# Kernel tuning notes

Measured on AMD Instinct MI355X. Metric: run time of the kernel, lower is better.

## Reference

```python
import jax, jax.numpy as jnp
import numpy as np

D3D, D2D, DTEXT, DPROJ, SEQ_LEN = 256, 768, 3072, 3072, 256
B, S, T = 32, 256, 512


def setup_inputs() -> dict:
    key = jax.random.key(0)
    ks = jax.random.split(key, 9)
    s3 = 1.0 / np.sqrt(D3D)
    s2 = 1.0 / np.sqrt(D2D)
    sf = 1.0 / np.sqrt(DPROJ * 3)
    return {
        "feat_3d": jax.random.normal(ks[0], (B, D3D), jnp.float32),
        "feat_2d": jax.random.normal(ks[1], (B, S, D2D), jnp.float32),
        "feat_text": jax.random.normal(ks[2], (B, T, DTEXT), jnp.float32),
        "W3d": jax.random.uniform(ks[3], (DPROJ, D3D), jnp.float32, -s3, s3),
        "b3d": jax.random.uniform(ks[4], (DPROJ,), jnp.float32, -s3, s3),
        "W2d": jax.random.uniform(ks[5], (DPROJ, D2D), jnp.float32, -s2, s2),
        "b2d": jax.random.uniform(ks[6], (DPROJ,), jnp.float32, -s2, s2),
        "Wf": jax.random.uniform(ks[7], (DPROJ, DPROJ * 3), jnp.float32, -sf, sf),
        "bf": jax.random.uniform(ks[8], (DPROJ,), jnp.float32, -sf, sf),
    }


def reference(feat_3d, feat_2d, feat_text, W3d, b3d, W2d, b2d, Wf, bf):
    # Projections
    f3p = feat_3d @ W3d.T + b3d                      # [B, P]
    f2p = jnp.einsum("bsd,pd->bsp", feat_2d, W2d) + b2d  # [B, S, P]

    # Attention pooling of 2D slice features against global 3D feature
    scores_s = jnp.einsum("bsp,bp->bs", f2p, f3p)    # [B, S]
    w_s = jax.nn.softmax(scores_s, axis=1)
    pooled_2d = jnp.einsum("bs,bsp->bp", w_s, f2p)   # [B, P]

    # Attention pooling of text features against global 3D feature
    scores_t = jnp.einsum("btp,bp->bt", feat_text, f3p)  # [B, T]
    w_t = jax.nn.softmax(scores_t, axis=1)
    pooled_text = jnp.einsum("bt,btp->bp", w_t, feat_text)  # [B, P]

    # All seq_len rows of the original's concatenated input are identical,
    # so compute the fusion GEMM once per batch element and broadcast.
    fused_vec = jnp.concatenate([f3p, pooled_2d, pooled_text], axis=-1) @ Wf.T + bf  # [B, P]
    return jnp.broadcast_to(fused_vec[:, None, :], (fused_vec.shape[0], SEQ_LEN, fused_vec.shape[1]))
```

## Files before the change

### kernel.cpp

```cpp
#include <hip/hip_runtime.h>

#define NB 32
#define NS 256
#define NT 512
#define KD3 256
#define KD2 768
#define NP 3072
#define KFZ 9216

__device__ __forceinline__ float wave_red_sum(float v) {
#pragma unroll
  for (int o = 32; o; o >>= 1) v += __shfl_xor(v, o, 64);
  return v;
}
__device__ __forceinline__ float wave_red_max(float v) {
#pragma unroll
  for (int o = 32; o; o >>= 1) v = fmaxf(v, __shfl_xor(v, o, 64));
  return v;
}

__global__ __launch_bounds__(256) void k1_f3p(const float* __restrict__ f3d,
                                              const float* __restrict__ W3d,
                                              const float* __restrict__ b3d,
                                              float* __restrict__ c0, float* __restrict__ c1,
                                              float* __restrict__ c2, float* __restrict__ c3) {
  int b = blockIdx.x & 31, pc = blockIdx.x >> 5;
  __shared__ float4 xs[KD3 / 4];
  int tid = threadIdx.x;
  if (tid < KD3 / 4) xs[tid] = ((const float4*)(f3d + b * KD3))[tid];
  __syncthreads();
  int p = pc * 256 + tid;
  const float4* wrow = (const float4*)(W3d + (size_t)p * KD3);
  float acc = b3d[p];
#pragma unroll 8
  for (int i = 0; i < KD3 / 4; ++i) {
    float4 w = wrow[i], x = xs[i];
    acc = fmaf(w.x, x.x, acc); acc = fmaf(w.y, x.y, acc);
    acc = fmaf(w.z, x.z, acc); acc = fmaf(w.w, x.w, acc);
  }
  size_t o = (size_t)b * KFZ + p;
  c0[o] = acc; c1[o] = 0.f; c2[o] = 0.f; c3[o] = 0.f;
}

__global__ __launch_bounds__(256) void k_L2(const float* __restrict__ ftx,
                                            const float* __restrict__ W2d,
                                            const float* __restrict__ c0,
                                            float* __restrict__ g_part,
                                            float* __restrict__ Pt,
                                            float* __restrict__ ml) {
  __shared__ float4 smem4[768];
  float* sm = (float*)smem4;
  int tid = threadIdx.x;
  if (blockIdx.x < 512) {
    int b = blockIdx.x & 31, tch = blockIdx.x >> 5;
    for (int i = tid; i < NP / 4; i += 256)
      smem4[i] = ((const float4*)(c0 + (size_t)b * KFZ))[i];
    __syncthreads();
    int wave = tid >> 6, lane = tid & 63;
    int t0 = tch * 32 + wave * 8;
    float m = -3.0e38f, l = 0.f;
    float4 acc[12];
#pragma unroll
    for (int j = 0; j < 12; ++j) acc[j] = make_float4(0.f, 0.f, 0.f, 0.f);
    for (int r = 0; r < 8; ++r) {
      const float4* row = (const float4*)(ftx + ((size_t)(b * NT + t0 + r)) * NP);
      float4 xr[12];
#pragma unroll
      for (int j = 0; j < 12; ++j) xr[j] = row[lane + 64 * j];
      float s = 0.f;
#pragma unroll
      for (int j = 0; j < 12; ++j) {
        float4 f = smem4[lane + 64 * j];
        s = fmaf(xr[j].x, f.x, s); s = fmaf(xr[j].y, f.y, s);
        s = fmaf(xr[j].z, f.z, s); s = fmaf(xr[j].w, f.w, s);
      }
      s = wave_red_sum(s);
      float mn = fmaxf(m, s);
      float al = __expf(m - mn);
      float e = __expf(s - mn);
      l = fmaf(l, al, e);
#pragma unroll
      for (int j = 0; j < 12; ++j) {
        acc[j].x = fmaf(acc[j].x, al, e * xr[j].x);
        acc[j].y = fmaf(acc[j].y, al, e * xr[j].y);
        acc[j].z = fmaf(acc[j].z, al, e * xr[j].z);
        acc[j].w = fmaf(acc[j].w, al, e * xr[j].w);
      }
      m = mn;
    }
    int c = tch * 4 + wave;
    float4* Pr = (float4*)(Pt + (size_t)(c * NB + b) * NP);
#pragma unroll
    for (int j = 0; j < 12; ++j) Pr[lane + 64 * j] = acc[j];
    if (lane == 0) { ml[(c * NB + b) * 2] = m; ml[(c * NB + b) * 2 + 1] = l; }
  } else {
    int id = blockIdx.x - 512;
    int dc = id % 3, kc = id / 3;
    int p0 = kc * 96;
    for (int i = tid; i < NB * 96; i += 256) {
      int bb = i / 96, pp = i - bb * 96;
      sm[i] = c0[(size_t)bb * KFZ + p0 + pp];
    }
    __syncthreads();
    int d = dc * 256 + tid;
    float acc[NB];
#pragma unroll
    for (int b = 0; b < NB; ++b) acc[b] = 0.f;
    for (int pp = 0; pp < 96; pp += 4) {
      float w0 = W2d[(size_t)(p0 + pp + 0) * KD2 + d];
      float w1 = W2d[(size_t)(p0 + pp + 1) * KD2 + d];
      float w2 = W2d[(size_t)(p0 + pp + 2) * KD2 + d];
      float w3 = W2d[(size_t)(p0 + pp + 3) * KD2 + d];
#pragma unroll
      for (int b = 0; b < NB; ++b) {
        float4 x4 = *(const float4*)&sm[b * 96 + pp];
        acc[b] = fmaf(w0, x4.x, acc[b]); acc[b] = fmaf(w1, x4.y, acc[b]);
        acc[b] = fmaf(w2, x4.z, acc[b]); acc[b] = fmaf(w3, x4.w, acc[b]);
      }
    }
#pragma unroll
    for (int b = 0; b < NB; ++b) g_part[(size_t)(kc * NB + b) * KD2 + d] = acc[b];
  }
}

__global__ __launch_bounds__(256) void k_L3(const float* __restrict__ f2d,
                                            const float* __restrict__ g_part,
                                            float* __restrict__ sraw,
                                            const float* __restrict__ Pt,
                                            const float* __restrict__ ml,
                                            float* __restrict__ c0, float* __restrict__ c1,
                                            float* __restrict__ c2, float* __restrict__ c3) {
  __shared__ float4 sh4[KD2 / 4];
  float* sh = (float*)sh4;
  int tid = threadIdx.x;
  if (blockIdx.x < 128) {
    int b = blockIdx.x & 31, sc = blockIdx.x >> 5;
    for (int i = tid; i < KD2; i += 256) {
      float a = 0.f;
      for (int c = 0; c < 32; ++c) a += g_part[(size_t)(c * NB + b) * KD2 + i];
      sh[i] = a;
    }
    __syncthreads();
    int wave = tid >> 6, lane = tid & 63;
    for (int i = 0; i < 16; ++i) {
      int s = sc * 64 + wave * 16 + i;
      const float4* row = (const float4*)(f2d + ((size_t)b * NS + s) * KD2);
      float acc = 0.f;
#pragma unroll
      for (int j = 0; j < 3; ++j) {
        float4 v = row[lane + 64 * j];
        float4 g = sh4[lane + 64 * j];
        acc = fmaf(v.x, g.x, acc); acc = fmaf(v.y, g.y, acc);
        acc = fmaf(v.z, g.z, acc); acc = fmaf(v.w, g.w, acc);
      }
      acc = wave_red_sum(acc);
      if (lane == 0) sraw[b * NS + s] = acc;
    }
  } else {
    int id = blockIdx.x - 128;
    int b = id & 31, pc = id >> 5;
    if (tid < 64) {
      sh[2 * tid] = ml[(tid * NB + b) * 2];
      sh[2 * tid + 1] = ml[(tid * NB + b) * 2 + 1];
    }
    __syncthreads();
    float M = -3.0e38f;
    for (int c = 0; c < 64; ++c) M = fmaxf(M, sh[2 * c]);
    float denom = 0.f;
    for (int c = 0; c < 64; ++c) denom += __expf(sh[2 * c] - M) * sh[2 * c + 1];
    float inv = 1.f / denom;
    int p4 = pc * 1024 + tid * 4;
    float4 a = make_float4(0.f, 0.f, 0.f, 0.f);
    for (int c = 0; c < 64; ++c) {
      float w = __expf(sh[2 * c] - M);
      float4 v = *(const float4*)&Pt[(size_t)(c * NB + b) * NP + p4];
      a.x = fmaf(w, v.x, a.x); a.y = fmaf(w, v.y, a.y);
      a.z = fmaf(w, v.z, a.z); a.w = fmaf(w, v.w, a.w);
    }
    a.x *= inv; a.y *= inv; a.z *= inv; a.w *= inv;
    size_t o = (size_t)b * KFZ + 2 * NP + p4;
    float4 z = make_float4(0.f, 0.f, 0.f, 0.f);
    *(float4*)&c0[o] = a;
    *(float4*)&c1[o] = z; *(float4*)&c2[o] = z; *(float4*)&c3[o] = z;
  }
}

__global__ __launch_bounds__(256) void k3c_sm(const float* __restrict__ f2d,
                                              const float* __restrict__ sraw,
                                              float* __restrict__ p2f) {
  int b = blockIdx.x & 31;
  int r = blockIdx.x >> 5;
  int dc = r % 3, sc = r / 3;
  __shared__ float pr[NS];
  __shared__ float red[8];
  int tid = threadIdx.x;
  int wave = tid >> 6, lane = tid & 63;
  float v = sraw[b * NS + tid];
  float mx = wave_red_max(v);
  if (lane == 0) red[wave] = mx;
  __syncthreads();
  float M = fmaxf(fmaxf(red[0], red[1]), fmaxf(red[2], red[3]));
  float e = __expf(v - M);
  pr[tid] = e;
  float smv = wave_red_sum(e);
  if (lane == 0) red[4 + wave] = smv;
  __syncthreads();
  float inv = 1.f / (red[4] + red[5] + red[6] + red[7]);
  int d = dc * 256 + tid;
  float acc = 0.f;
  const float* base = f2d + ((size_t)b * NS + sc * 128) * KD2 + d;
#pragma unroll 8
  for (int s = 0; s < 128; ++s)
    acc = fmaf(pr[sc * 128 + s], base[(size_t)s * KD2], acc);
  p2f[(size_t)(sc * NB + b) * KD2 + d] = acc * inv;
}

__global__ __launch_bounds__(256) void k5_pool2d(const float* __restrict__ W2d,
                                                 const float* __restrict__ b2d,
                                                 const float* __restrict__ p2f,
                                                 float* __restrict__ c0, float* __restrict__ c1,
                                                 float* __restrict__ c2, float* __restrict__ c3) {
  int pb = blockIdx.x >> 2, ks = blockIdx.x & 3;
  __shared__ __align__(16) float wt[64 * 68];
  __shared__ __align__(16) float xt[32 * 68];
  int tid = threadIdx.x;
  int tp = tid & 31, tb = tid >> 5;
  float acc[2][4];
#pragma unroll
  for (int i = 0; i < 2; ++i)
#pragma unroll
    for (int j = 0; j < 4; ++j) acc[i][j] = 0.f;
  for (int dk = 0; dk < 3; ++dk) {
    int d0 = ks * 192 + dk * 64;
#pragma unroll
    for (int it = 0; it < 4; ++it) {
      int idx = tid + it * 256;
      int row = idx >> 4, c4 = (idx & 15) * 4;
      *(float4*)&wt[row * 68 + c4] =
          *(const float4*)&W2d[(size_t)(pb * 64 + row) * KD2 + d0 + c4];
    }
#pragma unroll
    for (int it = 0; it < 2; ++it) {
      int idx = tid + it * 256;
      int row = idx >> 4, c4 = (idx & 15) * 4;
      float4 a = *(const float4*)&p2f[(size_t)row * KD2 + d0 + c4];
      float4 bq = *(const float4*)&p2f[(size_t)(NB + row) * KD2 + d0 + c4];
      a.x += bq.x; a.y += bq.y; a.z += bq.z; a.w += bq.w;
      *(float4*)&xt[row * 68 + c4] = a;
    }
    __syncthreads();
#pragma unroll 4
    for (int kk = 0; kk < 64; kk += 4) {
      float4 wv[2], xv[4];
#pragma unroll
      for (int i = 0; i < 2; ++i) wv[i] = *(const float4*)&wt[(tp + 32 * i) * 68 + kk];
#pragma unroll
      for (int j = 0; j < 4; ++j) xv[j] = *(const float4*)&xt[(tb + 8 * j) * 68 + kk];
#pragma unroll
      for (int i = 0; i < 2; ++i)
#pragma unroll
        for (int j = 0; j < 4; ++j) {
          acc[i][j] = fmaf(wv[i].x, xv[j].x, acc[i][j]);
          acc[i][j] = fmaf(wv[i].y, xv[j].y, acc[i][j]);
          acc[i][j] = fmaf(wv[i].z, xv[j].z, acc[i][j]);
          acc[i][j] = fmaf(wv[i].w, xv[j].w, acc[i][j]);
        }
    }
    __syncthreads();
  }
  float* dst = (ks == 0) ? c0 : (ks == 1) ? c1 : (ks == 2) ? c2 : c3;
#pragma unroll
  for (int i = 0; i < 2; ++i) {
    int p = pb * 64 + tp + 32 * i;
    float bias = (ks == 0) ? b2d[p] : 0.f;
#pragma unroll
    for (int j = 0; j < 4; ++j)
      dst[(size_t)(tb + 8 * j) * KFZ + NP + p] = acc[i][j] + bias;
  }
}

__global__ __launch_bounds__(256) void k6_fused(const float* __restrict__ Wf,
                                                const float* __restrict__ c0,
                                                const float* __restrict__ c1,
                                                const float* __restrict__ c2,
                                                const float* __restrict__ c3,
                                                float* __restrict__ fpart) {
  int pb = blockIdx.x >> 4, kc = blockIdx.x & 15;
  __shared__ __align__(16) float wt[192 * 68];
  __shared__ __align__(16) float xt[32 * 68];
  int tid = threadIdx.x;
  int tp = tid & 31, tb = tid >> 5;
  float acc[6][4];
#pragma unroll
  for (int i = 0; i < 6; ++i)
#pragma unroll
    for (int j = 0; j < 4; ++j) acc[i][j] = 0.f;
  for (int kt = 0; kt < 9; ++kt) {
    int k0 = kc * 576 + kt * 64;
#pragma unroll
    for (int it = 0; it < 12; ++it) {
      int idx = tid + it * 256;
      int row = idx >> 4, c4 = (idx & 15) * 4;
      *(float4*)&wt[row * 68 + c4] =
          *(const float4*)&Wf[(size_t)(pb * 192 + row) * KFZ + k0 + c4];
    }
#pragma unroll
    for (int it = 0; it < 2; ++it) {
      int idx = tid + it * 256;
      int row = idx >> 4, c4 = (idx & 15) * 4;
      size_t o = (size_t)row * KFZ + k0 + c4;
      float4 a = *(const float4*)&c0[o];
      float4 v1 = *(const float4*)&c1[o];
      float4 v2 = *(const float4*)&c2[o];
      float4 v3 = *(const float4*)&c3[o];
      a.x += v1.x + v2.x + v3.x; a.y += v1.y + v2.y + v3.y;
      a.z += v1.z + v2.z + v3.z; a.w += v1.w + v2.w + v3.w;
      *(float4*)&xt[row * 68 + c4] = a;
    }
    __syncthreads();
#pragma unroll 4
    for (int kk = 0; kk < 64; kk += 4) {
      float4 wv[6], xv[4];
#pragma unroll
      for (int i = 0; i < 6; ++i) wv[i] = *(const float4*)&wt[(tp + 32 * i) * 68 + kk];
#pragma unroll
      for (int j = 0; j < 4; ++j) xv[j] = *(const float4*)&xt[(tb + 8 * j) * 68 + kk];
#pragma unroll
      for (int i = 0; i < 6; ++i)
#pragma unroll
        for (int j = 0; j < 4; ++j) {
          acc[i][j] = fmaf(wv[i].x, xv[j].x, acc[i][j]);
          acc[i][j] = fmaf(wv[i].y, xv[j].y, acc[i][j]);
          acc[i][j] = fmaf(wv[i].z, xv[j].z, acc[i][j]);
          acc[i][j] = fmaf(wv[i].w, xv[j].w, acc[i][j]);
        }
    }
    __syncthreads();
  }
#pragma unroll
  for (int i = 0; i < 6; ++i)
#pragma unroll
    for (int j = 0; j < 4; ++j)
      fpart[(size_t)(kc * NB + tb + 8 * j) * NP + pb * 192 + tp + 32 * i] = acc[i][j];
}

__global__ __launch_bounds__(256) void k7_bcast(const float* __restrict__ fpart,
                                                const float* __restrict__ bfv,
                                                float* __restrict__ out) {
  int b = blockIdx.x & 31;
  int r = blockIdx.x >> 5;
  int pc = r % 3, sc = r / 3;
  int tid = threadIdx.x;
  int p4 = pc * 1024 + 4 * tid;
  float4 v = *(const float4*)&bfv[p4];
#pragma unroll
  for (int c = 0; c < 16; ++c) {
    float4 a = *(const float4*)&fpart[(size_t)(c * NB + b) * NP + p4];
    v.x += a.x; v.y += a.y; v.z += a.z; v.w += a.w;
  }
  float* obase = out + (size_t)b * NS * NP + p4;
  for (int ss = 0; ss < 64; ++ss) {
    int s = sc * 64 + ss;
    *(float4*)(obase + (size_t)s * NP) = v;
  }
}

extern "C" void kernel_launch(void* const* d_in, const int* in_sizes, int n_in,
                              void* d_out, int out_size, void* d_ws, size_t ws_size,
                              hipStream_t stream) {
  const float* f3d = (const float*)d_in[0];
  const float* f2d = (const float*)d_in[1];
  const float* ftx = (const float*)d_in[2];
  const float* W3d = (const float*)d_in[3];
  const float* b3d = (const float*)d_in[4];
  const float* W2d = (const float*)d_in[5];
  const float* b2d = (const float*)d_in[6];
  const float* Wf  = (const float*)d_in[7];
  const float* bfv = (const float*)d_in[8];
  float* out = (float*)d_out;
  float* ws = (float*)d_ws;

  float* c0     = ws;
  float* c1     = ws + 294912;
  float* c2     = ws + 589824;
  float* c3     = ws + 884736;
  float* g_part = ws + 1179648;
  float* sraw   = ws + 1966080;
  float* p2f    = ws + 1974272;
  float* ml     = ws + 2023424;
  float* Pt     = ws + 2027520;
  float* fpart  = ws + 8318976;

  k1_f3p<<<384, 256, 0, stream>>>(f3d, W3d, b3d, c0, c1, c2, c3);
  k_L2<<<608, 256, 0, stream>>>(ftx, W2d, c0, g_part, Pt, ml);
  k_L3<<<224, 256, 0, stream>>>(f2d, g_part, sraw, Pt, ml, c0, c1, c2, c3);
  k3c_sm<<<192, 256, 0, stream>>>(f2d, sraw, p2f);
  k5_pool2d<<<192, 256, 0, stream>>>(W2d, b2d, p2f, c0, c1, c2, c3);
  k6_fused<<<256, 256, 0, stream>>>(Wf, c0, c1, c2, c3, fpart);
  k7_bcast<<<384, 256, 0, stream>>>(fpart, bfv, out);
}
```

Baseline: 553.1 us.

## Split fused kernels, double-buffer text rows, and raise grid sizes across stages

The two multi-role kernels are split into separate text-attention, g-partial, score, and combine kernels. The text kernel now double-buffers row loads in registers and uses split accumulators. The 2D pooling, fusion GEMM, and broadcast kernels get finer partitions, so each launches more blocks. A separate pass pre-sums the four partial buffers before the fusion GEMM. This trades more kernel launches and extra memory passes for better overlap of loads and more occupancy on each stage.

```diff
diff --git a/kernel.cpp b/kernel.cpp
--- a/kernel.cpp
+++ b/kernel.cpp
@@ -42,147 +42,178 @@
   c0[o] = acc; c1[o] = 0.f; c2[o] = 0.f; c3[o] = 0.f;
 }
 
-__global__ __launch_bounds__(256) void k_L2(const float* __restrict__ ftx,
-                                            const float* __restrict__ W2d,
-                                            const float* __restrict__ c0,
-                                            float* __restrict__ g_part,
-                                            float* __restrict__ Pt,
-                                            float* __restrict__ ml) {
-  __shared__ float4 smem4[768];
-  float* sm = (float*)smem4;
-  int tid = threadIdx.x;
-  if (blockIdx.x < 512) {
-    int b = blockIdx.x & 31, tch = blockIdx.x >> 5;
-    for (int i = tid; i < NP / 4; i += 256)
-      smem4[i] = ((const float4*)(c0 + (size_t)b * KFZ))[i];
-    __syncthreads();
-    int wave = tid >> 6, lane = tid & 63;
-    int t0 = tch * 32 + wave * 8;
-    float m = -3.0e38f, l = 0.f;
-    float4 acc[12];
-#pragma unroll
-    for (int j = 0; j < 12; ++j) acc[j] = make_float4(0.f, 0.f, 0.f, 0.f);
-    for (int r = 0; r < 8; ++r) {
-      const float4* row = (const float4*)(ftx + ((size_t)(b * NT + t0 + r)) * NP);
-      float4 xr[12];
-#pragma unroll
-      for (int j = 0; j < 12; ++j) xr[j] = row[lane + 64 * j];
-      float s = 0.f;
-#pragma unroll
-      for (int j = 0; j < 12; ++j) {
-        float4 f = smem4[lane + 64 * j];
-        s = fmaf(xr[j].x, f.x, s); s = fmaf(xr[j].y, f.y, s);
-        s = fmaf(xr[j].z, f.z, s); s = fmaf(xr[j].w, f.w, s);
-      }
-      s = wave_red_sum(s);
-      float mn = fmaxf(m, s);
-      float al = __expf(m - mn);
-      float e = __expf(s - mn);
-      l = fmaf(l, al, e);
-#pragma unroll
-      for (int j = 0; j < 12; ++j) {
-        acc[j].x = fmaf(acc[j].x, al, e * xr[j].x);
-        acc[j].y = fmaf(acc[j].y, al, e * xr[j].y);
-        acc[j].z = fmaf(acc[j].z, al, e * xr[j].z);
-        acc[j].w = fmaf(acc[j].w, al, e * xr[j].w);
-      }
-      m = mn;
-    }
-    int c = tch * 4 + wave;
-    float4* Pr = (float4*)(Pt + (size_t)(c * NB + b) * NP);
-#pragma unroll
-    for (int j = 0; j < 12; ++j) Pr[lane + 64 * j] = acc[j];
-    if (lane == 0) { ml[(c * NB + b) * 2] = m; ml[(c * NB + b) * 2 + 1] = l; }
-  } else {
-    int id = blockIdx.x - 512;
-    int dc = id % 3, kc = id / 3;
-    int p0 = kc * 96;
-    for (int i = tid; i < NB * 96; i += 256) {
-      int bb = i / 96, pp = i - bb * 96;
-      sm[i] = c0[(size_t)bb * KFZ + p0 + pp];
-    }
-    __syncthreads();
-    int d = dc * 256 + tid;
-    float acc[NB];
-#pragma unroll
-    for (int b = 0; b < NB; ++b) acc[b] = 0.f;
-    for (int pp = 0; pp < 96; pp += 4) {
-      float w0 = W2d[(size_t)(p0 + pp + 0) * KD2 + d];
-      float w1 = W2d[(size_t)(p0 + pp + 1) * KD2 + d];
-      float w2 = W2d[(size_t)(p0 + pp + 2) * KD2 + d];
-      float w3 = W2d[(size_t)(p0 + pp + 3) * KD2 + d];
-#pragma unroll
-      for (int b = 0; b < NB; ++b) {
-        float4 x4 = *(const float4*)&sm[b * 96 + pp];
-        acc[b] = fmaf(w0, x4.x, acc[b]); acc[b] = fmaf(w1, x4.y, acc[b]);
-        acc[b] = fmaf(w2, x4.z, acc[b]); acc[b] = fmaf(w3, x4.w, acc[b]);
-      }
-    }
-#pragma unroll
-    for (int b = 0; b < NB; ++b) g_part[(size_t)(kc * NB + b) * KD2 + d] = acc[b];
-  }
-}
-
-__global__ __launch_bounds__(256) void k_L3(const float* __restrict__ f2d,
-                                            const float* __restrict__ g_part,
-                                            float* __restrict__ sraw,
-                                            const float* __restrict__ Pt,
-                                            const float* __restrict__ ml,
-                                            float* __restrict__ c0, float* __restrict__ c1,
-                                            float* __restrict__ c2, float* __restrict__ c3) {
-  __shared__ float4 sh4[KD2 / 4];
-  float* sh = (float*)sh4;
-  int tid = threadIdx.x;
-  if (blockIdx.x < 128) {
-    int b = blockIdx.x & 31, sc = blockIdx.x >> 5;
-    for (int i = tid; i < KD2; i += 256) {
-      float a = 0.f;
-      for (int c = 0; c < 32; ++c) a += g_part[(size_t)(c * NB + b) * KD2 + i];
-      sh[i] = a;
-    }
-    __syncthreads();
-    int wave = tid >> 6, lane = tid & 63;
-    for (int i = 0; i < 16; ++i) {
-      int s = sc * 64 + wave * 16 + i;
-      const float4* row = (const float4*)(f2d + ((size_t)b * NS + s) * KD2);
+__global__ __launch_bounds__(256, 2) void kT_text(const float* __restrict__ ftx,
+                                                  const float* __restrict__ c0,
+                                                  float* __restrict__ Pt,
+                                                  float* __restrict__ ml) {
+  int b = blockIdx.x & 31, tch = blockIdx.x >> 5;
+  __shared__ float4 f4[NP / 4];
+  int tid = threadIdx.x;
+#pragma unroll
+  for (int i = 0; i < 3; ++i)
+    f4[tid + 256 * i] = ((const float4*)(c0 + (size_t)b * KFZ))[tid + 256 * i];
+  __syncthreads();
+  int wave = tid >> 6, lane = tid & 63;
+  int t0 = tch * 32 + wave * 8;
+  const float4* rbase = (const float4*)(ftx + ((size_t)(b * NT + t0)) * NP);
+  float4 xa[12], xb[12];
+#pragma unroll
+  for (int j = 0; j < 12; ++j) xa[j] = rbase[lane + 64 * j];
+  float m = -3.0e38f, l = 0.f;
+  float4 acc[12];
+#pragma unroll
+  for (int j = 0; j < 12; ++j) acc[j] = make_float4(0.f, 0.f, 0.f, 0.f);
+#pragma unroll
+  for (int r = 0; r < 8; ++r) {
+    float4* cur = (r & 1) ? xb : xa;
+    float4* nxt = (r & 1) ? xa : xb;
+    if (r < 7) {
+      const float4* rn = rbase + (size_t)(r + 1) * (NP / 4);
+#pragma unroll
+      for (int j = 0; j < 12; ++j) nxt[j] = rn[lane + 64 * j];
+    }
+    float sx = 0.f, sy = 0.f, sz = 0.f, sw = 0.f;
+#pragma unroll
+    for (int j = 0; j < 12; ++j) {
+      float4 f = f4[lane + 64 * j];
+      sx = fmaf(cur[j].x, f.x, sx); sy = fmaf(cur[j].y, f.y, sy);
+      sz = fmaf(cur[j].z, f.z, sz); sw = fmaf(cur[j].w, f.w, sw);
+    }
+    float s = (sx + sy) + (sz + sw);
+    s = wave_red_sum(s);
+    float mn = fmaxf(m, s);
+    float al = __expf(m - mn);
+    float e = __expf(s - mn);
+    l = fmaf(l, al, e);
+#pragma unroll
+    for (int j = 0; j < 12; ++j) {
+      acc[j].x = fmaf(acc[j].x, al, e * cur[j].x);
+      acc[j].y = fmaf(acc[j].y, al, e * cur[j].y);
+      acc[j].z = fmaf(acc[j].z, al, e * cur[j].z);
+      acc[j].w = fmaf(acc[j].w, al, e * cur[j].w);
+    }
+    m = mn;
+  }
+  int c = tch * 4 + wave;
+  float4* Pr = (float4*)(Pt + (size_t)(c * NB + b) * NP);
+#pragma unroll
+  for (int j = 0; j < 12; ++j) Pr[lane + 64 * j] = acc[j];
+  if (lane == 0) { ml[(c * NB + b) * 2] = m; ml[(c * NB + b) * 2 + 1] = l; }
+}
+
+__global__ __launch_bounds__(256) void k2_gpart(const float* __restrict__ W2d,
+                                                const float* __restrict__ c0,
+                                                float* __restrict__ g_part) {
+  int dc = blockIdx.x % 3, kc = blockIdx.x / 3;
+  __shared__ float xs[NB * 96];
+  int tid = threadIdx.x;
+  int p0 = kc * 96;
+  for (int i = tid; i < NB * 96; i += 256) {
+    int bb = i / 96, pp = i - bb * 96;
+    xs[i] = c0[(size_t)bb * KFZ + p0 + pp];
+  }
+  __syncthreads();
+  int d = dc * 256 + tid;
+  float acc[NB];
+#pragma unroll
+  for (int b = 0; b < NB; ++b) acc[b] = 0.f;
+  for (int pp = 0; pp < 96; pp += 8) {
+    float w[8];
+#pragma unroll
+    for (int u = 0; u < 8; ++u) w[u] = W2d[(size_t)(p0 + pp + u) * KD2 + d];
+#pragma unroll
+    for (int b = 0; b < NB; ++b) {
+      float4 x0 = *(const float4*)&xs[b * 96 + pp];
+      float4 x1 = *(const float4*)&xs[b * 96 + pp + 4];
+      acc[b] = fmaf(w[0], x0.x, acc[b]); acc[b] = fmaf(w[1], x0.y, acc[b]);
+      acc[b] = fmaf(w[2], x0.z, acc[b]); acc[b] = fmaf(w[3], x0.w, acc[b]);
+      acc[b] = fmaf(w[4], x1.x, acc[b]); acc[b] = fmaf(w[5], x1.y, acc[b]);
+      acc[b] = fmaf(w[6], x1.z, acc[b]); acc[b] = fmaf(w[7], x1.w, acc[b]);
+    }
+  }
+#pragma unroll
+  for (int b = 0; b < NB; ++b) g_part[(size_t)(kc * NB + b) * KD2 + d] = acc[b];
+}
+
+__global__ __launch_bounds__(256) void k3a_scores(const float* __restrict__ f2d,
+                                                  const float* __restrict__ g_part,
+                                                  float* __restrict__ sraw) {
+  int b = blockIdx.x & 31, sc = blockIdx.x >> 5;
+  __shared__ float4 g4[KD2 / 4];
+  float* g = (float*)g4;
+  int tid = threadIdx.x;
+  for (int i = tid; i < KD2; i += 256) {
+    float a = 0.f;
+#pragma unroll 8
+    for (int c = 0; c < 32; ++c) a += g_part[(size_t)(c * NB + b) * KD2 + i];
+    g[i] = a;
+  }
+  __syncthreads();
+  int wave = tid >> 6, lane = tid & 63;
+#pragma unroll
+  for (int grp = 0; grp < 2; ++grp) {
+    int s0 = sc * 32 + wave * 8 + grp * 4;
+    float4 x[4][3];
+#pragma unroll
+    for (int rr = 0; rr < 4; ++rr) {
+      const float4* row = (const float4*)(f2d + ((size_t)b * NS + s0 + rr) * KD2);
+#pragma unroll
+      for (int j = 0; j < 3; ++j) x[rr][j] = row[lane + 64 * j];
+    }
+#pragma unroll
+    for (int rr = 0; rr < 4; ++rr) {
       float acc = 0.f;
 #pragma unroll
       for (int j = 0; j < 3; ++j) {
-        float4 v = row[lane + 64 * j];
-        float4 g = sh4[lane + 64 * j];
-        acc = fmaf(v.x, g.x, acc); acc = fmaf(v.y, g.y, acc);
-        acc = fmaf(v.z, g.z, acc); acc = fmaf(v.w, g.w, acc);
+        float4 f = g4[lane + 64 * j];
+        acc = fmaf(x[rr][j].x, f.x, acc); acc = fmaf(x[rr][j].y, f.y, acc);
+        acc = fmaf(x[rr][j].z, f.z, acc); acc = fmaf(x[rr][j].w, f.w, acc);
       }
       acc = wave_red_sum(acc);
-      if (lane == 0) sraw[b * NS + s] = acc;
-    }
-  } else {
-    int id = blockIdx.x - 128;
-    int b = id & 31, pc = id >> 5;
-    if (tid < 64) {
-      sh[2 * tid] = ml[(tid * NB + b) * 2];
-      sh[2 * tid + 1] = ml[(tid * NB + b) * 2 + 1];
-    }
-    __syncthreads();
-    float M = -3.0e38f;
-    for (int c = 0; c < 64; ++c) M = fmaxf(M, sh[2 * c]);
-    float denom = 0.f;
-    for (int c = 0; c < 64; ++c) denom += __expf(sh[2 * c] - M) * sh[2 * c + 1];
-    float inv = 1.f / denom;
-    int p4 = pc * 1024 + tid * 4;
-    float4 a = make_float4(0.f, 0.f, 0.f, 0.f);
-    for (int c = 0; c < 64; ++c) {
-      float w = __expf(sh[2 * c] - M);
-      float4 v = *(const float4*)&Pt[(size_t)(c * NB + b) * NP + p4];
-      a.x = fmaf(w, v.x, a.x); a.y = fmaf(w, v.y, a.y);
-      a.z = fmaf(w, v.z, a.z); a.w = fmaf(w, v.w, a.w);
-    }
-    a.x *= inv; a.y *= inv; a.z *= inv; a.w *= inv;
-    size_t o = (size_t)b * KFZ + 2 * NP + p4;
-    float4 z = make_float4(0.f, 0.f, 0.f, 0.f);
-    *(float4*)&c0[o] = a;
-    *(float4*)&c1[o] = z; *(float4*)&c2[o] = z; *(float4*)&c3[o] = z;
-  }
+      if (lane == 0) sraw[b * NS + s0 + rr] = acc;
+    }
+  }
+}
+
+__global__ __launch_bounds__(256) void kComb(const float* __restrict__ Pt,
+                                             const float* __restrict__ ml,
+                                             float* __restrict__ c0, float* __restrict__ c1,
+                                             float* __restrict__ c2, float* __restrict__ c3) {
+  int b = blockIdx.x & 31, pc = blockIdx.x >> 5;
+  __shared__ float sm[128];
+  int tid = threadIdx.x;
+  if (tid < 64) {
+    sm[tid] = ml[(tid * NB + b) * 2];
+    sm[64 + tid] = ml[(tid * NB + b) * 2 + 1];
+  }
+  __syncthreads();
+  float M = -3.0e38f;
+#pragma unroll 8
+  for (int c = 0; c < 64; ++c) M = fmaxf(M, sm[c]);
+  float denom = 0.f;
+#pragma unroll 8
+  for (int c = 0; c < 64; ++c) denom += __expf(sm[c] - M) * sm[64 + c];
+  float inv = 1.f / denom;
+  int p4 = pc * 1024 + tid * 4;
+  float4 a = make_float4(0.f, 0.f, 0.f, 0.f);
+#pragma unroll 2
+  for (int cg = 0; cg < 8; ++cg) {
+    float4 v[8];
+#pragma unroll
+    for (int u = 0; u < 8; ++u)
+      v[u] = *(const float4*)&Pt[(size_t)((cg * 8 + u) * NB + b) * NP + p4];
+#pragma unroll
+    for (int u = 0; u < 8; ++u) {
+      float w = __expf(sm[cg * 8 + u] - M);
+      a.x = fmaf(w, v[u].x, a.x); a.y = fmaf(w, v[u].y, a.y);
+      a.z = fmaf(w, v[u].z, a.z); a.w = fmaf(w, v[u].w, a.w);
+    }
+  }
+  a.x *= inv; a.y *= inv; a.z *= inv; a.w *= inv;
+  size_t o = (size_t)b * KFZ + 2 * NP + p4;
+  float4 z = make_float4(0.f, 0.f, 0.f, 0.f);
+  *(float4*)&c0[o] = a;
+  *(float4*)&c1[o] = z; *(float4*)&c2[o] = z; *(float4*)&c3[o] = z;
 }
 
 __global__ __launch_bounds__(256) void k3c_sm(const float* __restrict__ f2d,
@@ -208,10 +239,15 @@
   float inv = 1.f / (red[4] + red[5] + red[6] + red[7]);
   int d = dc * 256 + tid;
   float acc = 0.f;
-  const float* base = f2d + ((size_t)b * NS + sc * 128) * KD2 + d;
-#pragma unroll 8
-  for (int s = 0; s < 128; ++s)
-    acc = fmaf(pr[sc * 128 + s], base[(size_t)s * KD2], acc);
+  const float* base = f2d + ((size_t)b * NS + sc * 64) * KD2 + d;
+#pragma unroll 2
+  for (int sg = 0; sg < 8; ++sg) {
+    float xv[8];
+#pragma unroll
+    for (int u = 0; u < 8; ++u) xv[u] = base[(size_t)(sg * 8 + u) * KD2];
+#pragma unroll
+    for (int u = 0; u < 8; ++u) acc = fmaf(pr[sc * 64 + sg * 8 + u], xv[u], acc);
+  }
   p2f[(size_t)(sc * NB + b) * KD2 + d] = acc * inv;
 }
 
@@ -244,8 +280,11 @@
       int idx = tid + it * 256;
       int row = idx >> 4, c4 = (idx & 15) * 4;
       float4 a = *(const float4*)&p2f[(size_t)row * KD2 + d0 + c4];
-      float4 bq = *(const float4*)&p2f[(size_t)(NB + row) * KD2 + d0 + c4];
-      a.x += bq.x; a.y += bq.y; a.z += bq.z; a.w += bq.w;
+      float4 q1 = *(const float4*)&p2f[(size_t)(NB + row) * KD2 + d0 + c4];
+      float4 q2 = *(const float4*)&p2f[(size_t)(2 * NB + row) * KD2 + d0 + c4];
+      float4 q3 = *(const float4*)&p2f[(size_t)(3 * NB + row) * KD2 + d0 + c4];
+      a.x += q1.x + q2.x + q3.x; a.y += q1.y + q2.y + q3.y;
+      a.z += q1.z + q2.z + q3.z; a.w += q1.w + q2.w + q3.w;
       *(float4*)&xt[row * 68 + c4] = a;
     }
     __syncthreads();
@@ -279,54 +318,59 @@
   }
 }
 
+__global__ __launch_bounds__(256) void k_csum(float* __restrict__ c0,
+                                              const float* __restrict__ c1,
+                                              const float* __restrict__ c2,
+                                              const float* __restrict__ c3) {
+  int i = blockIdx.x * 256 + threadIdx.x;
+  float4 a = ((float4*)c0)[i];
+  float4 v1 = ((const float4*)c1)[i];
+  float4 v2 = ((const float4*)c2)[i];
+  float4 v3 = ((const float4*)c3)[i];
+  a.x += v1.x + v2.x + v3.x; a.y += v1.y + v2.y + v3.y;
+  a.z += v1.z + v2.z + v3.z; a.w += v1.w + v2.w + v3.w;
+  ((float4*)c0)[i] = a;
+}
+
 __global__ __launch_bounds__(256) void k6_fused(const float* __restrict__ Wf,
                                                 const float* __restrict__ c0,
-                                                const float* __restrict__ c1,
-                                                const float* __restrict__ c2,
-                                                const float* __restrict__ c3,
                                                 float* __restrict__ fpart) {
   int pb = blockIdx.x >> 4, kc = blockIdx.x & 15;
-  __shared__ __align__(16) float wt[192 * 68];
+  __shared__ __align__(16) float wt[96 * 68];
   __shared__ __align__(16) float xt[32 * 68];
   int tid = threadIdx.x;
   int tp = tid & 31, tb = tid >> 5;
-  float acc[6][4];
-#pragma unroll
-  for (int i = 0; i < 6; ++i)
+  float acc[3][4];
+#pragma unroll
+  for (int i = 0; i < 3; ++i)
 #pragma unroll
     for (int j = 0; j < 4; ++j) acc[i][j] = 0.f;
   for (int kt = 0; kt < 9; ++kt) {
     int k0 = kc * 576 + kt * 64;
 #pragma unroll
-    for (int it = 0; it < 12; ++it) {
+    for (int it = 0; it < 6; ++it) {
       int idx = tid + it * 256;
       int row = idx >> 4, c4 = (idx & 15) * 4;
       *(float4*)&wt[row * 68 + c4] =
-          *(const float4*)&Wf[(size_t)(pb * 192 + row) * KFZ + k0 + c4];
+          *(const float4*)&Wf[(size_t)(pb * 96 + row) * KFZ + k0 + c4];
     }
 #pragma unroll
     for (int it = 0; it < 2; ++it) {
       int idx = tid + it * 256;
       int row = idx >> 4, c4 = (idx & 15) * 4;
-      size_t o = (size_t)row * KFZ + k0 + c4;
-      float4 a = *(const float4*)&c0[o];
-      float4 v1 = *(const float4*)&c1[o];
-      float4 v2 = *(const float4*)&c2[o];
-      float4 v3 = *(const float4*)&c3[o];
-      a.x += v1.x + v2.x + v3.x; a.y += v1.y + v2.y + v3.y;
-      a.z += v1.z + v2.z + v3.z; a.w += v1.w + v2.w + v3.w;
-      *(float4*)&xt[row * 68 + c4] = a;
+      *(float4*)&xt[row * 68 + c4] =
+          *(const float4*)&c0[(size_t)row * KFZ + k0 + c4];
     }
     __syncthreads();
 #pragma unroll 4
     for (int kk = 0; kk < 64; kk += 4) {
-      float4 wv[6], xv[4];
-#pragma unroll
-      for (int i = 0; i < 6; ++i) wv[i] = *(const float4*)&wt[(tp + 32 * i) * 68 + kk];
+      float4 wv[3], xv[4];
+#pragma unroll
+      for (int i = 0; i < 3; ++i) wv[i] = *(const float4*)&wt[(tp + 32 * i) * 68 + kk];
 #pragma unroll
       for (int j = 0; j < 4; ++j) xv[j] = *(const float4*)&xt[(tb + 8 * j) * 68 + kk];
 #pragma unroll
-      for (int i = 0; i < 6; ++i)
+      for (int i = 0; i < 3; ++i)
 #pragma unroll
         for (int j = 0; j < 4; ++j) {
           acc[i][j] = fmaf(wv[i].x, xv[j].x, acc[i][j]);
@@ -338,10 +382,10 @@
     __syncthreads();
   }
 #pragma unroll
-  for (int i = 0; i < 6; ++i)
+  for (int i = 0; i < 3; ++i)
 #pragma unroll
     for (int j = 0; j < 4; ++j)
-      fpart[(size_t)(kc * NB + tb + 8 * j) * NP + pb * 192 + tp + 32 * i] = acc[i][j];
+      fpart[(size_t)(kc * NB + tb + 8 * j) * NP + pb * 96 + tp + 32 * i] = acc[i][j];
 }
 
 __global__ __launch_bounds__(256) void k7_bcast(const float* __restrict__ fpart,
@@ -359,8 +403,9 @@
     v.x += a.x; v.y += a.y; v.z += a.z; v.w += a.w;
   }
   float* obase = out + (size_t)b * NS * NP + p4;
-  for (int ss = 0; ss < 64; ++ss) {
-    int s = sc * 64 + ss;
+#pragma unroll 4
+  for (int ss = 0; ss < 32; ++ss) {
+    int s = sc * 32 + ss;
     *(float4*)(obase + (size_t)s * NP) = v;
   }
 }
@@ -387,15 +432,18 @@
   float* g_part = ws + 1179648;
   float* sraw   = ws + 1966080;
   float* p2f    = ws + 1974272;
-  float* ml     = ws + 2023424;
-  float* Pt     = ws + 2027520;
-  float* fpart  = ws + 8318976;
+  float* ml     = ws + 2072576;
+  float* Pt     = ws + 2076672;
+  float* fpart  = ws + 8368128;
 
   k1_f3p<<<384, 256, 0, stream>>>(f3d, W3d, b3d, c0, c1, c2, c3);
-  k_L2<<<608, 256, 0, stream>>>(ftx, W2d, c0, g_part, Pt, ml);
-  k_L3<<<224, 256, 0, stream>>>(f2d, g_part, sraw, Pt, ml, c0, c1, c2, c3);
-  k3c_sm<<<192, 256, 0, stream>>>(f2d, sraw, p2f);
+  kT_text<<<512, 256, 0, stream>>>(ftx, c0, Pt, ml);
+  k2_gpart<<<96, 256, 0, stream>>>(W2d, c0, g_part);
+  k3a_scores<<<256, 256, 0, stream>>>(f2d, g_part, sraw);
+  kComb<<<96, 256, 0, stream>>>(Pt, ml, c0, c1, c2, c3);
+  k3c_sm<<<384, 256, 0, stream>>>(f2d, sraw, p2f);
   k5_pool2d<<<192, 256, 0, stream>>>(W2d, b2d, p2f, c0, c1, c2, c3);
-  k6_fused<<<256, 256, 0, stream>>>(Wf, c0, c1, c2, c3, fpart);
-  k7_bcast<<<384, 256, 0, stream>>>(fpart, bfv, out);
-}
+  k_csum<<<288, 256, 0, stream>>>(c0, c1, c2, c3);
+  k6_fused<<<512, 256, 0, stream>>>(Wf, c0, fpart);
+  k7_bcast<<<768, 256, 0, stream>>>(fpart, bfv, out);
+}
```

Result: faster. 540.7 us (-2.2%).
